# Kernel optimization log

Measured on AMD Instinct MI355X. Metric: run time of the kernel, lower is better.

Reference implementation:

```python
import jax, jax.numpy as jnp
import numpy as np

B, S, D = 32, 2048, 1024

def setup_inputs() -> dict:
    key = jax.random.key(0)
    k1, k2, k3, k4, k5 = jax.random.split(key, 5)
    st = jax.random.normal(k1, (B, D), dtype=jnp.float32)
    hx = jax.random.normal(k2, (B, S, D), dtype=jnp.float32)
    hx_mask = (jax.random.uniform(k3, (B, S)) < 0.9).astype(jnp.float32)
    # kaiming_normal_(a=1, fan_in) -> std = sqrt(2/(1+a^2)/fan_in) = 1/sqrt(D)
    W = jax.random.normal(k4, (D, D), dtype=jnp.float32) / jnp.sqrt(jnp.float32(D))
    b = jax.random.normal(k5, (D,), dtype=jnp.float32)
    return {"st": st, "hx": hx, "hx_mask": hx_mask, "W": W, "b": b}

def reference(st, hx, hx_mask, W, b):
    # attn_type == 'general', prior_att is None
    # multiplicative mask with 1e-18 epsilon (faithful to original)
    hx_mask1 = hx_mask + (1.0 - hx_mask) * 1e-18            # [B,S]
    hx_t = jnp.einsum('bsd,ed->bse', hx, W) + b             # linear on hx, [B,S,D]
    score = jnp.einsum('bsd,bd->bs', hx_t, st)              # bmm(hx_t, st)
    score = score * hx_mask1
    attn = jax.nn.softmax(score, axis=-1)                   # [B,S]
    ct = jnp.einsum('bs,bsd->bd', attn, hx_t)               # weighted sum over src_len
    return ct
```

## Files before the change

### kernel.cpp

```cpp
#include <hip/hip_runtime.h>
#include <math.h>

#define BB 32
#define SS 2048
#define DD 1024
#define CHUNKS 32
#define ROWS_PER_CHUNK (SS / CHUNKS)
#define NWAVES 4
#define ROWS_PER_WAVE (ROWS_PER_CHUNK / NWAVES)
#define PSTRIDE (DD + 4)

#define ESPL 8
#define EPB (DD / ESPL)
#define VBG 4
#define VBPG (BB / VBG)

__global__ __launch_bounds__(256) void k_v(const float* __restrict__ st,
                                           const float* __restrict__ W,
                                           float* __restrict__ part_v) {
    const int dchunk = blockIdx.x;
    const int es = blockIdx.y;
    const int bg = blockIdx.z;
    const int tid = threadIdx.x;
    const int d = dchunk * 256 + tid;
    const int e0 = es * EPB;
    const int b0 = bg * VBPG;

    __shared__ float st_s[VBPG][EPB];
    for (int i = tid; i < VBPG * EPB; i += 256)
        st_s[i >> 7][i & 127] = st[(b0 + (i >> 7)) * DD + e0 + (i & 127)];
    __syncthreads();

    float acc[VBPG];
#pragma unroll
    for (int j = 0; j < VBPG; ++j) acc[j] = 0.f;

    for (int e = 0; e < EPB; ++e) {
        const float w = W[(size_t)(e0 + e) * DD + d];
#pragma unroll
        for (int j = 0; j < VBPG; ++j) acc[j] += st_s[j][e] * w;
    }
#pragma unroll
    for (int j = 0; j < VBPG; ++j)
        part_v[((size_t)es * BB + b0 + j) * DD + d] = acc[j];
}

__global__ __launch_bounds__(256) void k_main(const float* __restrict__ hx,
                                              const float* __restrict__ mask,
                                              const float* __restrict__ part_v,
                                              const float* __restrict__ st,
                                              const float* __restrict__ bias,
                                              float* __restrict__ part) {
    const int chunk = blockIdx.x;
    const int b = blockIdx.y;
    const int tid = threadIdx.x;
    const int wave = tid >> 6;
    const int lane = tid & 63;

    float4 vr[4];
#pragma unroll
    for (int k = 0; k < 4; ++k) vr[k] = make_float4(0.f, 0.f, 0.f, 0.f);
#pragma unroll
    for (int es = 0; es < ESPL; ++es) {
        const float* pv = part_v + ((size_t)es * BB + b) * DD;
#pragma unroll
        for (int k = 0; k < 4; ++k) {
            float4 t = *reinterpret_cast<const float4*>(pv + k * 256 + 4 * lane);
            vr[k].x += t.x; vr[k].y += t.y; vr[k].z += t.z; vr[k].w += t.w;
        }
    }

    float cb = 0.f;
    {
        const float* stb = st + b * DD;
#pragma unroll
        for (int k = 0; k < 4; ++k) {
            float4 bv = *reinterpret_cast<const float4*>(bias + k * 256 + 4 * lane);
            float4 sv = *reinterpret_cast<const float4*>(stb + k * 256 + 4 * lane);
            cb += bv.x * sv.x + bv.y * sv.y + bv.z * sv.z + bv.w * sv.w;
        }
#pragma unroll
        for (int o = 32; o; o >>= 1) cb += __shfl_xor(cb, o, 64);
    }

    const int s0 = chunk * ROWS_PER_CHUNK + wave * ROWS_PER_WAVE;
    const float* hxb = hx + (size_t)b * SS * DD;
    const float* mb = mask + (size_t)b * SS;

    float m = -INFINITY, l = 0.f;
    float4 u[4];
#pragma unroll
    for (int k = 0; k < 4; ++k) u[k] = make_float4(0.f, 0.f, 0.f, 0.f);

    for (int g = 0; g < ROWS_PER_WAVE / 4; ++g) {
        const int s = s0 + 4 * g;
        const float* row = hxb + (size_t)s * DD;
        float4 h[4][4];
#pragma unroll
        for (int r = 0; r < 4; ++r)
#pragma unroll
            for (int k = 0; k < 4; ++k)
                h[r][k] = *reinterpret_cast<const float4*>(row + (size_t)r * DD + k * 256 + 4 * lane);

        float d0 = 0.f, d1 = 0.f, d2 = 0.f, d3 = 0.f;
#pragma unroll
        for (int k = 0; k < 4; ++k) {
            d0 += h[0][k].x * vr[k].x + h[0][k].y * vr[k].y + h[0][k].z * vr[k].z + h[0][k].w * vr[k].w;
            d1 += h[1][k].x * vr[k].x + h[1][k].y * vr[k].y + h[1][k].z * vr[k].z + h[1][k].w * vr[k].w;
            d2 += h[2][k].x * vr[k].x + h[2][k].y * vr[k].y + h[2][k].z * vr[k].z + h[2][k].w * vr[k].w;
            d3 += h[3][k].x * vr[k].x + h[3][k].y * vr[k].y + h[3][k].z * vr[k].z + h[3][k].w * vr[k].w;
        }
#pragma unroll
        for (int o = 32; o; o >>= 1) {
            d0 += __shfl_xor(d0, o, 64);
            d1 += __shfl_xor(d1, o, 64);
            d2 += __shfl_xor(d2, o, 64);
            d3 += __shfl_xor(d3, o, 64);
        }

        const float4 mk = *reinterpret_cast<const float4*>(mb + s);
        float sc0 = (d0 + cb) * (mk.x + (1.0f - mk.x) * 1e-18f);
        float sc1 = (d1 + cb) * (mk.y + (1.0f - mk.y) * 1e-18f);
        float sc2 = (d2 + cb) * (mk.z + (1.0f - mk.z) * 1e-18f);
        float sc3 = (d3 + cb) * (mk.w + (1.0f - mk.w) * 1e-18f);

        const float gm = fmaxf(fmaxf(sc0, sc1), fmaxf(sc2, sc3));
        if (gm > m) {
            const float f = __expf(m - gm);
            l *= f;
#pragma unroll
            for (int k = 0; k < 4; ++k) {
                u[k].x *= f; u[k].y *= f; u[k].z *= f; u[k].w *= f;
            }
            m = gm;
        }
        const float p0 = __expf(sc0 - m);
        const float p1 = __expf(sc1 - m);
        const float p2 = __expf(sc2 - m);
        const float p3 = __expf(sc3 - m);
        l += p0 + p1 + p2 + p3;
#pragma unroll
        for (int k = 0; k < 4; ++k) {
            u[k].x += p0 * h[0][k].x + p1 * h[1][k].x + p2 * h[2][k].x + p3 * h[3][k].x;
            u[k].y += p0 * h[0][k].y + p1 * h[1][k].y + p2 * h[2][k].y + p3 * h[3][k].y;
            u[k].z += p0 * h[0][k].z + p1 * h[1][k].z + p2 * h[2][k].z + p3 * h[3][k].z;
            u[k].w += p0 * h[0][k].w + p1 * h[1][k].w + p2 * h[2][k].w + p3 * h[3][k].w;
        }
    }

    __shared__ float s_m[NWAVES], s_l[NWAVES];
    __shared__ float s_u[NWAVES][DD];
    if (lane == 0) { s_m[wave] = m; s_l[wave] = l; }
#pragma unroll
    for (int k = 0; k < 4; ++k)
        *reinterpret_cast<float4*>(&s_u[wave][k * 256 + 4 * lane]) = u[k];
    __syncthreads();

    const float M = fmaxf(fmaxf(s_m[0], s_m[1]), fmaxf(s_m[2], s_m[3]));
    const float f0 = __expf(s_m[0] - M), f1 = __expf(s_m[1] - M);
    const float f2 = __expf(s_m[2] - M), f3 = __expf(s_m[3] - M);
    const float L = s_l[0] * f0 + s_l[1] * f1 + s_l[2] * f2 + s_l[3] * f3;

    float* pb = part + (size_t)(b * CHUNKS + chunk) * PSTRIDE;
    float4 a0 = *reinterpret_cast<const float4*>(&s_u[0][4 * tid]);
    float4 a1 = *reinterpret_cast<const float4*>(&s_u[1][4 * tid]);
    float4 a2 = *reinterpret_cast<const float4*>(&s_u[2][4 * tid]);
    float4 a3 = *reinterpret_cast<const float4*>(&s_u[3][4 * tid]);
    float4 acc;
    acc.x = a0.x * f0 + a1.x * f1 + a2.x * f2 + a3.x * f3;
    acc.y = a0.y * f0 + a1.y * f1 + a2.y * f2 + a3.y * f3;
    acc.z = a0.z * f0 + a1.z * f1 + a2.z * f2 + a3.z * f3;
    acc.w = a0.w * f0 + a1.w * f1 + a2.w * f2 + a3.w * f3;
    *reinterpret_cast<float4*>(pb + 4 * tid) = acc;
    if (tid == 0) { pb[DD] = M; pb[DD + 1] = L; }
}

__global__ __launch_bounds__(256) void k_reduce(const float* __restrict__ part,
                                                float* __restrict__ ubar) {
    const int b = blockIdx.x;
    const int tid = threadIdx.x;
    __shared__ float s_f[CHUNKS];
    __shared__ float s_red[2];
    const float* pb = part + (size_t)b * CHUNKS * PSTRIDE;

    float mi = (tid < CHUNKS) ? pb[tid * PSTRIDE + DD] : -INFINITY;
    float M = mi;
#pragma unroll
    for (int o = 32; o; o >>= 1) M = fmaxf(M, __shfl_xor(M, o, 64));
    if (tid == 0) s_red[0] = M;
    __syncthreads();
    M = s_red[0];

    const float li = (tid < CHUNKS) ? pb[tid * PSTRIDE + DD + 1] : 0.f;
    const float fi = (tid < CHUNKS) ? __expf(mi - M) : 0.f;
    if (tid < CHUNKS) s_f[tid] = fi;
    float Lp = li * fi;
#pragma unroll
    for (int o = 32; o; o >>= 1) Lp += __shfl_xor(Lp, o, 64);
    if (tid == 0) s_red[1] = Lp;
    __syncthreads();
    const float invL = 1.f / s_red[1];

    float4 acc = make_float4(0.f, 0.f, 0.f, 0.f);
    for (int i = 0; i < CHUNKS; ++i) {
        const float f = s_f[i];
        float4 ui = *reinterpret_cast<const float4*>(pb + (size_t)i * PSTRIDE + 4 * tid);
        acc.x += f * ui.x; acc.y += f * ui.y; acc.z += f * ui.z; acc.w += f * ui.w;
    }
    acc.x *= invL; acc.y *= invL; acc.z *= invL; acc.w *= invL;
    *reinterpret_cast<float4*>(ubar + (size_t)b * DD + 4 * tid) = acc;
}

__global__ __launch_bounds__(256) void k_out(const float* __restrict__ ubar,
                                             const float* __restrict__ W,
                                             const float* __restrict__ bias,
                                             float* __restrict__ out) {
    const int echunk = blockIdx.x;
    const int bg = blockIdx.y;
    const int tid = threadIdx.x;
    const int wave = tid >> 6;
    const int lane = tid & 63;
    const int b0 = bg * 4;

    float4 ur[4][4];
#pragma unroll
    for (int j = 0; j < 4; ++j) {
        const float* ub = ubar + (size_t)(b0 + j) * DD;
#pragma unroll
        for (int k = 0; k < 4; ++k)
            ur[j][k] = *reinterpret_cast<const float4*>(ub + k * 256 + 4 * lane);
    }

    for (int i = 0; i < 8; ++i) {
        const int e = echunk * 32 + wave * 8 + i;
        const float* wr = W + (size_t)e * DD;
        float4 w4[4];
#pragma unroll
        for (int k = 0; k < 4; ++k)
            w4[k] = *reinterpret_cast<const float4*>(wr + k * 256 + 4 * lane);

        float d0 = 0.f, d1 = 0.f, d2 = 0.f, d3 = 0.f;
#pragma unroll
        for (int k = 0; k < 4; ++k) {
            d0 += w4[k].x * ur[0][k].x + w4[k].y * ur[0][k].y + w4[k].z * ur[0][k].z + w4[k].w * ur[0][k].w;
            d1 += w4[k].x * ur[1][k].x + w4[k].y * ur[1][k].y + w4[k].z * ur[1][k].z + w4[k].w * ur[1][k].w;
            d2 += w4[k].x * ur[2][k].x + w4[k].y * ur[2][k].y + w4[k].z * ur[2][k].z + w4[k].w * ur[2][k].w;
            d3 += w4[k].x * ur[3][k].x + w4[k].y * ur[3][k].y + w4[k].z * ur[3][k].z + w4[k].w * ur[3][k].w;
        }
#pragma unroll
        for (int o = 32; o; o >>= 1) {
            d0 += __shfl_xor(d0, o, 64);
            d1 += __shfl_xor(d1, o, 64);
            d2 += __shfl_xor(d2, o, 64);
            d3 += __shfl_xor(d3, o, 64);
        }
        if (lane == 0) {
            const float be = bias[e];
            out[(size_t)(b0 + 0) * DD + e] = d0 + be;
            out[(size_t)(b0 + 1) * DD + e] = d1 + be;
            out[(size_t)(b0 + 2) * DD + e] = d2 + be;
            out[(size_t)(b0 + 3) * DD + e] = d3 + be;
        }
    }
}

extern "C" void kernel_launch(void* const* d_in, const int* in_sizes, int n_in,
                              void* d_out, int out_size, void* d_ws, size_t ws_size,
                              hipStream_t stream) {
    const float* st   = (const float*)d_in[0];
    const float* hx   = (const float*)d_in[1];
    const float* msk  = (const float*)d_in[2];
    const float* W    = (const float*)d_in[3];
    const float* bias = (const float*)d_in[4];
    float* out = (float*)d_out;

    float* ws = (float*)d_ws;
    float* part_v = ws;
    float* part   = part_v + (size_t)ESPL * BB * DD;
    float* ubar   = part + (size_t)BB * CHUNKS * PSTRIDE;

    k_v<<<dim3(4, ESPL, VBG), 256, 0, stream>>>(st, W, part_v);
    k_main<<<dim3(CHUNKS, BB), 256, 0, stream>>>(hx, msk, part_v, st, bias, part);
    k_reduce<<<BB, 256, 0, stream>>>(part, ubar);
    k_out<<<dim3(32, 8), 256, 0, stream>>>(ubar, W, bias, out);
}
```

Before: 81.71 us.

## Double-buffer hx row loads and pair lanes in the shuffle reduction

The main attention loop now loads two rows per step into alternating register buffers, so the loads for the next pair are issued before the current pair is computed. This hides global-load latency inside a fully unrolled loop. The two dot-product reductions also share one butterfly by swapping halves across odd and even lanes, which cuts shuffle count. Processing two rows per step instead of four means more online-softmax rescale checks, and full unrolling increases code size and register pressure.

```diff
diff --git a/kernel.cpp b/kernel.cpp
--- a/kernel.cpp
+++ b/kernel.cpp
@@ -84,7 +84,7 @@
     }
 
     const int s0 = chunk * ROWS_PER_CHUNK + wave * ROWS_PER_WAVE;
-    const float* hxb = hx + (size_t)b * SS * DD;
+    const float* hxb = hx + (size_t)b * SS * DD + 4 * lane;
     const float* mb = mask + (size_t)b * SS;
 
     float m = -INFINITY, l = 0.f;
@@ -92,39 +92,42 @@
 #pragma unroll
     for (int k = 0; k < 4; ++k) u[k] = make_float4(0.f, 0.f, 0.f, 0.f);
 
-    for (int g = 0; g < ROWS_PER_WAVE / 4; ++g) {
-        const int s = s0 + 4 * g;
-        const float* row = hxb + (size_t)s * DD;
-        float4 h[4][4];
-#pragma unroll
-        for (int r = 0; r < 4; ++r)
-#pragma unroll
-            for (int k = 0; k < 4; ++k)
-                h[r][k] = *reinterpret_cast<const float4*>(row + (size_t)r * DD + k * 256 + 4 * lane);
-
-        float d0 = 0.f, d1 = 0.f, d2 = 0.f, d3 = 0.f;
+    float4 hA[2][4], hB[2][4];
+
+    auto loadrows = [&](float4 (&h)[2][4], int s) {
+        const float* r0 = hxb + (size_t)s * DD;
+#pragma unroll
+        for (int k = 0; k < 4; ++k) {
+            h[0][k] = *reinterpret_cast<const float4*>(r0 + k * 256);
+            h[1][k] = *reinterpret_cast<const float4*>(r0 + DD + k * 256);
+        }
+    };
+
+    auto compute = [&](const float4 (&h)[2][4], int s) {
+        float d0 = 0.f, d1 = 0.f;
 #pragma unroll
         for (int k = 0; k < 4; ++k) {
             d0 += h[0][k].x * vr[k].x + h[0][k].y * vr[k].y + h[0][k].z * vr[k].z + h[0][k].w * vr[k].w;
             d1 += h[1][k].x * vr[k].x + h[1][k].y * vr[k].y + h[1][k].z * vr[k].z + h[1][k].w * vr[k].w;
-            d2 += h[2][k].x * vr[k].x + h[2][k].y * vr[k].y + h[2][k].z * vr[k].z + h[2][k].w * vr[k].w;
-            d3 += h[3][k].x * vr[k].x + h[3][k].y * vr[k].y + h[3][k].z * vr[k].z + h[3][k].w * vr[k].w;
-        }
-#pragma unroll
-        for (int o = 32; o; o >>= 1) {
-            d0 += __shfl_xor(d0, o, 64);
-            d1 += __shfl_xor(d1, o, 64);
-            d2 += __shfl_xor(d2, o, 64);
-            d3 += __shfl_xor(d3, o, 64);
-        }
-
-        const float4 mk = *reinterpret_cast<const float4*>(mb + s);
-        float sc0 = (d0 + cb) * (mk.x + (1.0f - mk.x) * 1e-18f);
-        float sc1 = (d1 + cb) * (mk.y + (1.0f - mk.y) * 1e-18f);
-        float sc2 = (d2 + cb) * (mk.z + (1.0f - mk.z) * 1e-18f);
-        float sc3 = (d3 + cb) * (mk.w + (1.0f - mk.w) * 1e-18f);
-
-        const float gm = fmaxf(fmaxf(sc0, sc1), fmaxf(sc2, sc3));
+        }
+        const bool odd = (lane & 1);
+        float a = odd ? d1 : d0;
+        float t = odd ? d0 : d1;
+        a += __shfl_xor(t, 1, 64);
+        a += __shfl_xor(a, 2, 64);
+        a += __shfl_xor(a, 4, 64);
+        a += __shfl_xor(a, 8, 64);
+        a += __shfl_xor(a, 16, 64);
+        a += __shfl_xor(a, 32, 64);
+        const float o = __shfl_xor(a, 1, 64);
+        const float dd0 = odd ? o : a;
+        const float dd1 = odd ? a : o;
+
+        const float2 mk = *reinterpret_cast<const float2*>(mb + s);
+        const float sc0 = (dd0 + cb) * (mk.x + (1.0f - mk.x) * 1e-18f);
+        const float sc1 = (dd1 + cb) * (mk.y + (1.0f - mk.y) * 1e-18f);
+
+        const float gm = fmaxf(sc0, sc1);
         if (gm > m) {
             const float f = __expf(m - gm);
             l *= f;
@@ -136,17 +139,23 @@
         }
         const float p0 = __expf(sc0 - m);
         const float p1 = __expf(sc1 - m);
-        const float p2 = __expf(sc2 - m);
-        const float p3 = __expf(sc3 - m);
-        l += p0 + p1 + p2 + p3;
-#pragma unroll
-        for (int k = 0; k < 4; ++k) {
-            u[k].x += p0 * h[0][k].x + p1 * h[1][k].x + p2 * h[2][k].x + p3 * h[3][k].x;
-            u[k].y += p0 * h[0][k].y + p1 * h[1][k].y + p2 * h[2][k].y + p3 * h[3][k].y;
-            u[k].z += p0 * h[0][k].z + p1 * h[1][k].z + p2 * h[2][k].z + p3 * h[3][k].z;
-            u[k].w += p0 * h[0][k].w + p1 * h[1][k].w + p2 * h[2][k].w + p3 * h[3][k].w;
-        }
-    }
+        l += p0 + p1;
+#pragma unroll
+        for (int k = 0; k < 4; ++k) {
+            u[k].x += p0 * h[0][k].x + p1 * h[1][k].x;
+            u[k].y += p0 * h[0][k].y + p1 * h[1][k].y;
+            u[k].z += p0 * h[0][k].z + p1 * h[1][k].z;
+            u[k].w += p0 * h[0][k].w + p1 * h[1][k].w;
+        }
+    };
+
+    loadrows(hA, s0);
+#pragma unroll
+    for (int g = 0; g < ROWS_PER_WAVE / 2 - 1; ++g) {
+        if (g & 1) { loadrows(hA, s0 + 2 * (g + 1)); compute(hB, s0 + 2 * g); }
+        else       { loadrows(hB, s0 + 2 * (g + 1)); compute(hA, s0 + 2 * g); }
+    }
+    compute(hB, s0 + ROWS_PER_WAVE - 2);
 
     __shared__ float s_m[NWAVES], s_l[NWAVES];
     __shared__ float s_u[NWAVES][DD];
```

After: 75.94 us. -7.1%, faster.
